# Kernel optimization log

Hardware: AMD Instinct MI355X
Metric: run time of the kernel (lower is better)

Reference implementation:

```python
import jax, jax.numpy as jnp
import numpy as np

B, L, D = 2048, 200, 128
HID = [80, 40]


def setup_inputs() -> dict:
    key = jax.random.key(0)
    ks = jax.random.split(key, 10)
    hist_emb = jax.random.normal(ks[0], (B, L, D), dtype=jnp.float32)
    target_emb = jax.random.normal(ks[1], (B, D), dtype=jnp.float32)
    mask = jax.random.randint(ks[2], (B, L), 0, 2, dtype=jnp.int32)
    # MLP params: (4D -> 80 -> 40 -> 1), Kaiming-uniform-ish like nn.Linear default
    dims = [4 * D] + HID + [1]
    params = {}
    for i in range(len(dims) - 1):
        fan_in = dims[i]
        bound = 1.0 / np.sqrt(fan_in)
        params[f"W{i}"] = jax.random.uniform(ks[3 + 2 * i], (dims[i], dims[i + 1]), minval=-bound, maxval=bound, dtype=jnp.float32)
        params[f"b{i}"] = jax.random.uniform(ks[4 + 2 * i], (dims[i + 1],), minval=-bound, maxval=bound, dtype=jnp.float32)
    return {"hist_emb": hist_emb, "target_emb": target_emb, "mask": mask, **params}


def reference(hist_emb, target_emb, mask, W0, b0, W1, b1, W2, b2):
    # hist_emb: (B,L,D); target_emb: (B,D); mask: (B,L)
    target = target_emb[:, None, :]                       # (B,1,D) -> broadcast over L
    diff = hist_emb - target
    prod = hist_emb * target
    tgt = jnp.broadcast_to(target, hist_emb.shape)
    feat = jnp.concatenate([hist_emb, tgt, diff, prod], axis=-1)  # (B,L,4D)
    h = jax.nn.relu(jnp.einsum("blf,fh->blh", feat, W0) + b0)
    h = jax.nn.relu(jnp.einsum("blf,fh->blh", h, W1) + b1)
    scores = (jnp.einsum("blf,fh->blh", h, W2) + b2)[..., 0]      # (B,L)
    m = mask.astype(scores.dtype)
    logits = scores + (1.0 - m) * -1e9
    attn = jax.nn.softmax(logits, axis=1)                 # (B,L)
    user_interest = jnp.einsum("bl,bld->bd", attn, hist_emb)
    return user_interest, attn
```

## Files before the change

kernel.cpp:

```cpp
#include <hip/hip_runtime.h>
#include <hip/hip_bf16.h>

#define B_  2048
#define L_  200
#define D_  128
#define H0_ 80
#define H1_ 40
#define BPB 4
#define NTILE 13
#define TT_ (BPB*NTILE)

#define WS_BG  0
#define WS_W1T 20480
#define WS_W0P 25088
#define WS_TOT 35840

typedef __attribute__((ext_vector_type(8))) short short8;
typedef __attribute__((ext_vector_type(4))) float floatx4;

__device__ __forceinline__ short f2bf(float f) {
    unsigned u = __float_as_uint(f);
    u += 0x7fffu + ((u >> 16) & 1u);
    return (short)(u >> 16);
}
__device__ __forceinline__ float bf2f(short s) {
    return __uint_as_float(((unsigned)(unsigned short)s) << 16);
}

__global__ __launch_bounds__(256) void prep_kernel(
    const float* __restrict__ W0, const float* __restrict__ W1,
    short* __restrict__ ws)
{
    for (int i = blockIdx.x * 256 + threadIdx.x; i < WS_TOT; i += 64 * 256) {
        short v;
        if (i < WS_W1T) {
            int h = i >> 8, k = i & 255;
            float x = (k < 128) ? (W0[(size_t)k * H0_ + h] + W0[(size_t)(256 + k) * H0_ + h])
                                : W0[(size_t)(384 + (k - 128)) * H0_ + h];
            v = f2bf(x);
        } else if (i < WS_W0P) {
            int j = i - WS_W1T;
            int n = j / 96, k = j - n * 96;
            v = (n < H1_ && k < H0_) ? f2bf(W1[(size_t)k * H1_ + n]) : (short)0;
        } else {
            int j = i - WS_W0P;
            int d = j / 84, h = j - d * 84;
            v = (h < H0_) ? f2bf(W0[(size_t)(128 + d) * H0_ + h] - W0[(size_t)(256 + d) * H0_ + h])
                          : (short)0;
        }
        ws[i] = v;
    }
}

__global__ __launch_bounds__(256, 2) void fused_kernel(
    const float* __restrict__ hist, const float* __restrict__ tgt,
    const int* __restrict__ mask, const short* __restrict__ ws,
    const float* __restrict__ b0p, const float* __restrict__ b1,
    const float* __restrict__ W2, const float* __restrict__ b2,
    float* __restrict__ out)
{
    __shared__ __align__(16) short Bs[H0_][264];
    __shared__ __align__(16) short h0t[4][16][104];
    __shared__ float tgs4[BPB][D_];
    __shared__ float beffs[BPB][H0_];
    __shared__ float scores4[BPB][208];
    __shared__ float red[8];
    __shared__ float p0[D_], p1[D_];

    const int tid = threadIdx.x;
    const int wave = tid >> 6, lane = tid & 63;
    const int col = lane & 15, quad = lane >> 4;
    const int bbase = blockIdx.x * BPB;

    short* w0s = &Bs[0][0];
    float* red3 = &scores4[0][0];

    for (int i = tid; i < 1344; i += 256)
        *(short8*)(w0s + i * 8) = *(const short8*)(ws + WS_W0P + i * 8);
    for (int i = tid; i < BPB * D_; i += 256)
        tgs4[i >> 7][i & 127] = tgt[(size_t)(bbase + (i >> 7)) * D_ + (i & 127)];
    __syncthreads();

    for (int bb = 0; bb < BPB; ++bb) {
        if (tid < 240) {
            int seg = tid / 80, h = tid - seg * 80;
            int d0 = seg * 43, d1 = (seg == 2) ? D_ : d0 + 43;
            float s = 0.f;
            #pragma unroll 8
            for (int d = d0; d < d1; ++d) s += tgs4[bb][d] * bf2f(w0s[d * 84 + h]);
            red3[seg * H0_ + h] = s;
        }
        __syncthreads();
        if (tid < H0_)
            beffs[bb][tid] = b0p[tid] + red3[tid] + red3[H0_ + tid] + red3[2 * H0_ + tid];
        __syncthreads();
    }

    for (int i = tid; i < 2560; i += 256) {
        int h = i >> 5, k0 = (i & 31) * 8;
        *(short8*)&Bs[h][k0] = *(const short8*)(ws + WS_BG + (h << 8) + k0);
    }
    if (tid < 192) {
        int w = tid / 48, rem = tid % 48, row = rem / 3, c = 80 + (rem % 3) * 8;
        *(short8*)&h0t[w][row][c] = (short8)0;
    }
    short8 w1f[3][3];
    #pragma unroll
    for (int ks = 0; ks < 3; ++ks)
        #pragma unroll
        for (int nt = 0; nt < 3; ++nt)
            w1f[ks][nt] = *(const short8*)(ws + WS_W1T + (nt * 16 + col) * 96 + ks * 32 + quad * 8);
    float b1r[3], w2r[3];
    #pragma unroll
    for (int nt = 0; nt < 3; ++nt) {
        int h = nt * 16 + col;
        b1r[nt] = (h < H1_) ? b1[h] : 0.f;
        w2r[nt] = (h < H1_) ? W2[h] : 0.f;
    }
    const float b2v = b2[0];
    __syncthreads();

    for (int tt = wave; tt < TT_; tt += 4) {
        const int bb = tt / NTILE, t = tt - bb * NTILE;
        const int l = t * 16 + col;
        const int lc = (l < L_) ? l : (L_ - 1);
        const float* ap = hist + ((size_t)(bbase + bb) * L_ + lc) * D_ + quad * 8;

        floatx4 A[8], T8[8];
        #pragma unroll
        for (int u = 0; u < 8; ++u) A[u] = *(const floatx4*)(ap + (u >> 1) * 32 + (u & 1) * 4);
        #pragma unroll
        for (int u = 0; u < 8; ++u)
            T8[u] = *(const floatx4*)&tgs4[bb][quad * 8 + (u >> 1) * 32 + (u & 1) * 4];

        short8 ah[4], ag[4];
        #pragma unroll
        for (int ks = 0; ks < 4; ++ks) {
            short8 h8, g8;
            #pragma unroll
            for (int j = 0; j < 8; ++j) {
                float hv = A[2 * ks + (j >> 2)][j & 3];
                float tv = T8[2 * ks + (j >> 2)][j & 3];
                h8[j] = f2bf(hv);
                g8[j] = f2bf(hv * tv);
            }
            ah[ks] = h8; ag[ks] = g8;
        }

        floatx4 c0[5];
        #pragma unroll
        for (int nt = 0; nt < 5; ++nt) c0[nt] = (floatx4)0.f;
        #pragma unroll
        for (int ks = 0; ks < 4; ++ks)
            #pragma unroll
            for (int nt = 0; nt < 5; ++nt) {
                short8 bfr = *(const short8*)&Bs[nt * 16 + col][ks * 32 + quad * 8];
                c0[nt] = __builtin_amdgcn_mfma_f32_16x16x32_bf16(ah[ks], bfr, c0[nt], 0, 0, 0);
            }
        #pragma unroll
        for (int ks = 0; ks < 4; ++ks)
            #pragma unroll
            for (int nt = 0; nt < 5; ++nt) {
                short8 bfr = *(const short8*)&Bs[nt * 16 + col][128 + ks * 32 + quad * 8];
                c0[nt] = __builtin_amdgcn_mfma_f32_16x16x32_bf16(ag[ks], bfr, c0[nt], 0, 0, 0);
            }

        #pragma unroll
        for (int nt = 0; nt < 5; ++nt) {
            float be = beffs[bb][nt * 16 + col];
            #pragma unroll
            for (int r = 0; r < 4; ++r) {
                float v = c0[nt][r] + be;
                v = v > 0.f ? v : 0.f;
                h0t[wave][quad * 4 + r][nt * 16 + col] = f2bf(v);
            }
        }

        floatx4 c1[3];
        #pragma unroll
        for (int nt = 0; nt < 3; ++nt) c1[nt] = (floatx4)0.f;
        #pragma unroll
        for (int ks = 0; ks < 3; ++ks) {
            short8 a1 = *(const short8*)&h0t[wave][col][ks * 32 + quad * 8];
            #pragma unroll
            for (int nt = 0; nt < 3; ++nt)
                c1[nt] = __builtin_amdgcn_mfma_f32_16x16x32_bf16(a1, w1f[ks][nt], c1[nt], 0, 0, 0);
        }

        float s4[4] = {0.f, 0.f, 0.f, 0.f};
        #pragma unroll
        for (int nt = 0; nt < 3; ++nt)
            #pragma unroll
            for (int r = 0; r < 4; ++r) {
                float v = c1[nt][r] + b1r[nt];
                v = v > 0.f ? v : 0.f;
                s4[r] += v * w2r[nt];
            }
        #pragma unroll
        for (int r = 0; r < 4; ++r) {
            s4[r] += __shfl_xor(s4[r], 1, 16);
            s4[r] += __shfl_xor(s4[r], 2, 16);
            s4[r] += __shfl_xor(s4[r], 4, 16);
            s4[r] += __shfl_xor(s4[r], 8, 16);
        }
        if (col == 0) {
            #pragma unroll
            for (int r = 0; r < 4; ++r)
                scores4[bb][t * 16 + quad * 4 + r] = s4[r] + b2v;
        }
    }
    __syncthreads();

    for (int bb = 0; bb < BPB; ++bb) {
        const int b = bbase + bb;

        float sc = -3.0e38f;
        if (tid < L_) {
            sc = scores4[bb][tid];
            if (mask[(size_t)b * L_ + tid] == 0) sc -= 1e9f;
        }
        float m = sc;
        #pragma unroll
        for (int off = 32; off >= 1; off >>= 1) m = fmaxf(m, __shfl_xor(m, off, 64));
        if (lane == 0) red[wave] = m;
        __syncthreads();
        m = fmaxf(fmaxf(red[0], red[1]), fmaxf(red[2], red[3]));
        float e = (tid < L_) ? __expf(sc - m) : 0.f;
        float s = e;
        #pragma unroll
        for (int off = 32; off >= 1; off >>= 1) s += __shfl_xor(s, off, 64);
        if (lane == 0) red[4 + wave] = s;
        __syncthreads();
        s = red[4] + red[5] + red[6] + red[7];
        float av = e * (1.0f / s);
        if (tid < L_) {
            scores4[bb][tid] = av;
            out[(size_t)B_ * D_ + (size_t)b * L_ + tid] = av;
        }
        __syncthreads();

        const int half = tid >> 7, d = tid & 127;
        const float* hb = hist + ((size_t)b * L_ + half * 100) * D_ + d;
        float acc = 0.f;
        #pragma unroll 25
        for (int l = 0; l < 100; ++l)
            acc = fmaf(scores4[bb][half * 100 + l], hb[(size_t)l * D_], acc);
        if (half) p1[d] = acc; else p0[d] = acc;
        __syncthreads();
        if (tid < D_) out[(size_t)b * D_ + tid] = p0[tid] + p1[tid];
    }
}

extern "C" void kernel_launch(void* const* d_in, const int* in_sizes, int n_in,
                              void* d_out, int out_size, void* d_ws, size_t ws_size,
                              hipStream_t stream) {
    const float* hist = (const float*)d_in[0];
    const float* tgt  = (const float*)d_in[1];
    const int*   mask = (const int*)d_in[2];
    const float* W0   = (const float*)d_in[3];
    const float* b0   = (const float*)d_in[4];
    const float* W1   = (const float*)d_in[5];
    const float* b1   = (const float*)d_in[6];
    const float* W2   = (const float*)d_in[7];
    const float* b2   = (const float*)d_in[8];

    short* ws = (short*)d_ws;

    prep_kernel<<<64, 256, 0, stream>>>(W0, W1, ws);
    fused_kernel<<<B_ / BPB, 256, 0, stream>>>(hist, tgt, mask, ws, b0, b1, W2, b2,
                                               (float*)d_out);
}
```

Measured before the change: 362.1 us.

## Fold target into per-batch W0 to halve first-layer MFMAs, raise occupancy

Each batch row's target vector is folded into an effective first-layer weight (Wa + t*Wd) built in shared memory, so layer 0 needs only the hist operand and half the MFMAs per tile. Batches per block drop from 4 to 2 and launch bounds rise to 4 blocks per CU, with a smaller shared-memory footprint. The softmax and weighted sum are rewritten so each wave pair handles one batch with fewer barriers and float2 loads. In exchange, the weight matrix is rebuilt per batch with a barrier each time, and folding t into the bf16 weights adds rounding error.

```diff
diff --git a/kernel.cpp b/kernel.cpp
--- a/kernel.cpp
+++ b/kernel.cpp
@@ -6,9 +6,8 @@
 #define D_  128
 #define H0_ 80
 #define H1_ 40
-#define BPB 4
+#define BPB 2
 #define NTILE 13
-#define TT_ (BPB*NTILE)
 
 #define WS_BG  0
 #define WS_W1T 20480
@@ -17,6 +16,7 @@
 
 typedef __attribute__((ext_vector_type(8))) short short8;
 typedef __attribute__((ext_vector_type(4))) float floatx4;
+typedef __attribute__((ext_vector_type(2))) float floatx2;
 
 __device__ __forceinline__ short f2bf(float f) {
     unsigned u = __float_as_uint(f);
@@ -52,56 +52,30 @@
     }
 }
 
-__global__ __launch_bounds__(256, 2) void fused_kernel(
+__global__ __launch_bounds__(256, 4) void fused_kernel(
     const float* __restrict__ hist, const float* __restrict__ tgt,
     const int* __restrict__ mask, const short* __restrict__ ws,
     const float* __restrict__ b0p, const float* __restrict__ b1,
     const float* __restrict__ W2, const float* __restrict__ b2,
     float* __restrict__ out)
 {
-    __shared__ __align__(16) short Bs[H0_][264];
-    __shared__ __align__(16) short h0t[4][16][104];
+    __shared__ __align__(16) short wbuf[10752];
+    __shared__ __align__(16) short h0t[4][16][100];
     __shared__ float tgs4[BPB][D_];
     __shared__ float beffs[BPB][H0_];
     __shared__ float scores4[BPB][208];
-    __shared__ float red[8];
-    __shared__ float p0[D_], p1[D_];
 
     const int tid = threadIdx.x;
     const int wave = tid >> 6, lane = tid & 63;
     const int col = lane & 15, quad = lane >> 4;
     const int bbase = blockIdx.x * BPB;
 
-    short* w0s = &Bs[0][0];
-    float* red3 = &scores4[0][0];
-
     for (int i = tid; i < 1344; i += 256)
-        *(short8*)(w0s + i * 8) = *(const short8*)(ws + WS_W0P + i * 8);
+        *(short8*)(wbuf + i * 8) = *(const short8*)(ws + WS_W0P + i * 8);
     for (int i = tid; i < BPB * D_; i += 256)
         tgs4[i >> 7][i & 127] = tgt[(size_t)(bbase + (i >> 7)) * D_ + (i & 127)];
-    __syncthreads();
-
-    for (int bb = 0; bb < BPB; ++bb) {
-        if (tid < 240) {
-            int seg = tid / 80, h = tid - seg * 80;
-            int d0 = seg * 43, d1 = (seg == 2) ? D_ : d0 + 43;
-            float s = 0.f;
-            #pragma unroll 8
-            for (int d = d0; d < d1; ++d) s += tgs4[bb][d] * bf2f(w0s[d * 84 + h]);
-            red3[seg * H0_ + h] = s;
-        }
-        __syncthreads();
-        if (tid < H0_)
-            beffs[bb][tid] = b0p[tid] + red3[tid] + red3[H0_ + tid] + red3[2 * H0_ + tid];
-        __syncthreads();
-    }
-
-    for (int i = tid; i < 2560; i += 256) {
-        int h = i >> 5, k0 = (i & 31) * 8;
-        *(short8*)&Bs[h][k0] = *(const short8*)(ws + WS_BG + (h << 8) + k0);
-    }
-    if (tid < 192) {
-        int w = tid / 48, rem = tid % 48, row = rem / 3, c = 80 + (rem % 3) * 8;
+    if (tid < 128) {
+        int w = tid >> 5, row = (tid >> 1) & 15, c = 80 + (tid & 1) * 8;
         *(short8*)&h0t[w][row][c] = (short8)0;
     }
     short8 w1f[3][3];
@@ -120,134 +94,168 @@
     const float b2v = b2[0];
     __syncthreads();
 
-    for (int tt = wave; tt < TT_; tt += 4) {
-        const int bb = tt / NTILE, t = tt - bb * NTILE;
-        const int l = t * 16 + col;
-        const int lc = (l < L_) ? l : (L_ - 1);
-        const float* ap = hist + ((size_t)(bbase + bb) * L_ + lc) * D_ + quad * 8;
-
-        floatx4 A[8], T8[8];
-        #pragma unroll
-        for (int u = 0; u < 8; ++u) A[u] = *(const floatx4*)(ap + (u >> 1) * 32 + (u & 1) * 4);
-        #pragma unroll
-        for (int u = 0; u < 8; ++u)
-            T8[u] = *(const floatx4*)&tgs4[bb][quad * 8 + (u >> 1) * 32 + (u & 1) * 4];
-
-        short8 ah[4], ag[4];
-        #pragma unroll
-        for (int ks = 0; ks < 4; ++ks) {
-            short8 h8, g8;
-            #pragma unroll
-            for (int j = 0; j < 8; ++j) {
-                float hv = A[2 * ks + (j >> 2)][j & 3];
-                float tv = T8[2 * ks + (j >> 2)][j & 3];
-                h8[j] = f2bf(hv);
-                g8[j] = f2bf(hv * tv);
-            }
-            ah[ks] = h8; ag[ks] = g8;
-        }
-
-        floatx4 c0[5];
-        #pragma unroll
-        for (int nt = 0; nt < 5; ++nt) c0[nt] = (floatx4)0.f;
-        #pragma unroll
-        for (int ks = 0; ks < 4; ++ks)
+    if (tid < 160) {
+        int bb = tid >= 80 ? 1 : 0, h = tid - bb * 80;
+        float s = 0.f;
+        #pragma unroll 8
+        for (int d = 0; d < D_; ++d) s += tgs4[bb][d] * bf2f(wbuf[d * 84 + h]);
+        beffs[bb][h] = b0p[h] + s;
+    }
+    __syncthreads();
+
+    for (int bb = 0; bb < BPB; ++bb) {
+        for (int i = tid; i < 1280; i += 256) {
+            int h = i >> 4, d0 = (i & 15) * 8;
+            short8 wa = *(const short8*)(ws + WS_BG + h * 256 + d0);
+            short8 wd = *(const short8*)(ws + WS_BG + h * 256 + 128 + d0);
+            floatx4 t0 = *(const floatx4*)&tgs4[bb][d0];
+            floatx4 t1 = *(const floatx4*)&tgs4[bb][d0 + 4];
+            short8 o;
+            #pragma unroll
+            for (int j = 0; j < 4; ++j) o[j] = f2bf(bf2f(wa[j]) + t0[j] * bf2f(wd[j]));
+            #pragma unroll
+            for (int j = 4; j < 8; ++j) o[j] = f2bf(bf2f(wa[j]) + t1[j - 4] * bf2f(wd[j]));
+            *(short8*)(wbuf + h * 132 + d0) = o;
+        }
+        __syncthreads();
+
+        const int b = bbase + bb;
+        for (int t = (wave + bb) & 3; t < NTILE; t += 4) {
+            const int l = t * 16 + col;
+            const int lc = (l < L_) ? l : (L_ - 1);
+            const float* ap = hist + ((size_t)b * L_ + lc) * D_ + quad * 8;
+
+            floatx4 A[8];
+            #pragma unroll
+            for (int u = 0; u < 8; ++u)
+                A[u] = *(const floatx4*)(ap + (u >> 1) * 32 + (u & 1) * 4);
+
+            short8 ah[4];
+            #pragma unroll
+            for (int ks = 0; ks < 4; ++ks) {
+                short8 h8;
+                #pragma unroll
+                for (int j = 0; j < 8; ++j) h8[j] = f2bf(A[2 * ks + (j >> 2)][j & 3]);
+                ah[ks] = h8;
+            }
+
+            floatx4 c0[5];
+            #pragma unroll
+            for (int nt = 0; nt < 5; ++nt) c0[nt] = (floatx4)0.f;
+            #pragma unroll
+            for (int ks = 0; ks < 4; ++ks)
+                #pragma unroll
+                for (int nt = 0; nt < 5; ++nt) {
+                    short8 bfr = *(const short8*)(wbuf + (nt * 16 + col) * 132 + ks * 32 + quad * 8);
+                    c0[nt] = __builtin_amdgcn_mfma_f32_16x16x32_bf16(ah[ks], bfr, c0[nt], 0, 0, 0);
+                }
+
             #pragma unroll
             for (int nt = 0; nt < 5; ++nt) {
-                short8 bfr = *(const short8*)&Bs[nt * 16 + col][ks * 32 + quad * 8];
-                c0[nt] = __builtin_amdgcn_mfma_f32_16x16x32_bf16(ah[ks], bfr, c0[nt], 0, 0, 0);
-            }
-        #pragma unroll
-        for (int ks = 0; ks < 4; ++ks)
-            #pragma unroll
-            for (int nt = 0; nt < 5; ++nt) {
-                short8 bfr = *(const short8*)&Bs[nt * 16 + col][128 + ks * 32 + quad * 8];
-                c0[nt] = __builtin_amdgcn_mfma_f32_16x16x32_bf16(ag[ks], bfr, c0[nt], 0, 0, 0);
-            }
-
-        #pragma unroll
-        for (int nt = 0; nt < 5; ++nt) {
-            float be = beffs[bb][nt * 16 + col];
+                float be = beffs[bb][nt * 16 + col];
+                #pragma unroll
+                for (int r = 0; r < 4; ++r) {
+                    float v = c0[nt][r] + be;
+                    v = v > 0.f ? v : 0.f;
+                    h0t[wave][quad * 4 + r][nt * 16 + col] = f2bf(v);
+                }
+            }
+
+            floatx4 c1[3];
+            #pragma unroll
+            for (int nt = 0; nt < 3; ++nt) c1[nt] = (floatx4)0.f;
+            #pragma unroll
+            for (int ks = 0; ks < 3; ++ks) {
+                short8 a1 = *(const short8*)&h0t[wave][col][ks * 32 + quad * 8];
+                #pragma unroll
+                for (int nt = 0; nt < 3; ++nt)
+                    c1[nt] = __builtin_amdgcn_mfma_f32_16x16x32_bf16(a1, w1f[ks][nt], c1[nt], 0, 0, 0);
+            }
+
+            float s4[4] = {0.f, 0.f, 0.f, 0.f};
+            #pragma unroll
+            for (int nt = 0; nt < 3; ++nt)
+                #pragma unroll
+                for (int r = 0; r < 4; ++r) {
+                    float v = c1[nt][r] + b1r[nt];
+                    v = v > 0.f ? v : 0.f;
+                    s4[r] += v * w2r[nt];
+                }
             #pragma unroll
             for (int r = 0; r < 4; ++r) {
-                float v = c0[nt][r] + be;
-                v = v > 0.f ? v : 0.f;
-                h0t[wave][quad * 4 + r][nt * 16 + col] = f2bf(v);
-            }
-        }
-
-        floatx4 c1[3];
-        #pragma unroll
-        for (int nt = 0; nt < 3; ++nt) c1[nt] = (floatx4)0.f;
-        #pragma unroll
-        for (int ks = 0; ks < 3; ++ks) {
-            short8 a1 = *(const short8*)&h0t[wave][col][ks * 32 + quad * 8];
-            #pragma unroll
-            for (int nt = 0; nt < 3; ++nt)
-                c1[nt] = __builtin_amdgcn_mfma_f32_16x16x32_bf16(a1, w1f[ks][nt], c1[nt], 0, 0, 0);
-        }
-
-        float s4[4] = {0.f, 0.f, 0.f, 0.f};
-        #pragma unroll
-        for (int nt = 0; nt < 3; ++nt)
-            #pragma unroll
-            for (int r = 0; r < 4; ++r) {
-                float v = c1[nt][r] + b1r[nt];
-                v = v > 0.f ? v : 0.f;
-                s4[r] += v * w2r[nt];
-            }
-        #pragma unroll
-        for (int r = 0; r < 4; ++r) {
-            s4[r] += __shfl_xor(s4[r], 1, 16);
-            s4[r] += __shfl_xor(s4[r], 2, 16);
-            s4[r] += __shfl_xor(s4[r], 4, 16);
-            s4[r] += __shfl_xor(s4[r], 8, 16);
-        }
-        if (col == 0) {
-            #pragma unroll
-            for (int r = 0; r < 4; ++r)
-                scores4[bb][t * 16 + quad * 4 + r] = s4[r] + b2v;
-        }
-    }
-    __syncthreads();
-
-    for (int bb = 0; bb < BPB; ++bb) {
-        const int b = bbase + bb;
-
-        float sc = -3.0e38f;
-        if (tid < L_) {
-            sc = scores4[bb][tid];
-            if (mask[(size_t)b * L_ + tid] == 0) sc -= 1e9f;
-        }
-        float m = sc;
+                s4[r] += __shfl_xor(s4[r], 1, 16);
+                s4[r] += __shfl_xor(s4[r], 2, 16);
+                s4[r] += __shfl_xor(s4[r], 4, 16);
+                s4[r] += __shfl_xor(s4[r], 8, 16);
+            }
+            if (col == 0) {
+                #pragma unroll
+                for (int r = 0; r < 4; ++r)
+                    scores4[bb][t * 16 + quad * 4 + r] = s4[r] + b2v;
+            }
+        }
+        __syncthreads();
+    }
+
+    float* pw = (float*)&h0t[0][0][0];
+    float* attn_w = pw + 4 * 128;
+    {
+        const int bb = wave >> 1, b = bbase + bb, half = wave & 1;
+        float sc[4], e[4];
+        float m = -3.0e38f;
+        #pragma unroll
+        for (int j = 0; j < 4; ++j) {
+            int idx = lane + 64 * j;
+            if (idx < L_) {
+                float v = scores4[bb][idx];
+                if (mask[(size_t)b * L_ + idx] == 0) v -= 1e9f;
+                sc[j] = v;
+                m = fmaxf(m, v);
+            } else sc[j] = -3.0e38f;
+        }
         #pragma unroll
         for (int off = 32; off >= 1; off >>= 1) m = fmaxf(m, __shfl_xor(m, off, 64));
-        if (lane == 0) red[wave] = m;
-        __syncthreads();
-        m = fmaxf(fmaxf(red[0], red[1]), fmaxf(red[2], red[3]));
-        float e = (tid < L_) ? __expf(sc - m) : 0.f;
-        float s = e;
+        float s = 0.f;
+        #pragma unroll
+        for (int j = 0; j < 4; ++j) {
+            int idx = lane + 64 * j;
+            e[j] = (idx < L_) ? __expf(sc[j] - m) : 0.f;
+            s += e[j];
+        }
         #pragma unroll
         for (int off = 32; off >= 1; off >>= 1) s += __shfl_xor(s, off, 64);
-        if (lane == 0) red[4 + wave] = s;
-        __syncthreads();
-        s = red[4] + red[5] + red[6] + red[7];
-        float av = e * (1.0f / s);
-        if (tid < L_) {
-            scores4[bb][tid] = av;
-            out[(size_t)B_ * D_ + (size_t)b * L_ + tid] = av;
-        }
-        __syncthreads();
-
-        const int half = tid >> 7, d = tid & 127;
-        const float* hb = hist + ((size_t)b * L_ + half * 100) * D_ + d;
-        float acc = 0.f;
+        float inv = 1.0f / s;
+        if (half == 0) {
+            #pragma unroll
+            for (int j = 0; j < 4; ++j) {
+                int idx = lane + 64 * j;
+                if (idx < L_) {
+                    float av = e[j] * inv;
+                    attn_w[bb * 200 + idx] = av;
+                    out[(size_t)B_ * D_ + (size_t)b * L_ + idx] = av;
+                }
+            }
+        }
+    }
+    __syncthreads();
+    {
+        const int bb = wave >> 1, b = bbase + bb, half = wave & 1;
+        const int d2 = lane * 2;
+        const float* hb = hist + ((size_t)b * L_ + half * 100) * D_ + d2;
+        float a0 = 0.f, a1 = 0.f;
         #pragma unroll 25
-        for (int l = 0; l < 100; ++l)
-            acc = fmaf(scores4[bb][half * 100 + l], hb[(size_t)l * D_], acc);
-        if (half) p1[d] = acc; else p0[d] = acc;
-        __syncthreads();
-        if (tid < D_) out[(size_t)b * D_ + tid] = p0[tid] + p1[tid];
+        for (int l = 0; l < 100; ++l) {
+            float w = attn_w[bb * 200 + half * 100 + l];
+            floatx2 h2 = *(const floatx2*)(hb + (size_t)l * D_);
+            a0 = fmaf(w, h2.x, a0);
+            a1 = fmaf(w, h2.y, a1);
+        }
+        *(floatx2*)&pw[wave * 128 + d2] = floatx2{a0, a1};
+    }
+    __syncthreads();
+    {
+        int bp = tid >> 7, d = tid & 127;
+        out[(size_t)(bbase + bp) * D_ + d] = pw[(bp * 2) * 128 + d] + pw[(bp * 2 + 1) * 128 + d];
     }
 }
 
```

Result: slower. 403.1 us (+11.3%).

## Fold target product into per-batch W0 fragments and prefetch history tiles

Applied to the files above, without the earlier changes.

Since the target is constant within a batch row, the hist*target block of W0 is folded into an effective per-batch weight (W_a + t*W_d) built in registers. This halves the first-layer MFMA count and removes the shared-memory weight tile. The first-layer bias is now computed by looping over all 128 dimensions from global memory in one pass, replacing the segmented reduction and two syncs per batch. The tile loop is restructured per batch with a staggered start and register prefetch of the next history tile. The cost is extra register pressure from 20 weight fragments plus the prefetch buffer, and a second bf16 rounding of the effective weights.

```diff
diff --git a/kernel.cpp b/kernel.cpp
--- a/kernel.cpp
+++ b/kernel.cpp
@@ -8,7 +8,6 @@
 #define H1_ 40
 #define BPB 4
 #define NTILE 13
-#define TT_ (BPB*NTILE)
 
 #define WS_BG  0
 #define WS_W1T 20480
@@ -59,7 +58,6 @@
     const float* __restrict__ W2, const float* __restrict__ b2,
     float* __restrict__ out)
 {
-    __shared__ __align__(16) short Bs[H0_][264];
     __shared__ __align__(16) short h0t[4][16][104];
     __shared__ float tgs4[BPB][D_];
     __shared__ float beffs[BPB][H0_];
@@ -72,34 +70,8 @@
     const int col = lane & 15, quad = lane >> 4;
     const int bbase = blockIdx.x * BPB;
 
-    short* w0s = &Bs[0][0];
-    float* red3 = &scores4[0][0];
-
-    for (int i = tid; i < 1344; i += 256)
-        *(short8*)(w0s + i * 8) = *(const short8*)(ws + WS_W0P + i * 8);
     for (int i = tid; i < BPB * D_; i += 256)
         tgs4[i >> 7][i & 127] = tgt[(size_t)(bbase + (i >> 7)) * D_ + (i & 127)];
-    __syncthreads();
-
-    for (int bb = 0; bb < BPB; ++bb) {
-        if (tid < 240) {
-            int seg = tid / 80, h = tid - seg * 80;
-            int d0 = seg * 43, d1 = (seg == 2) ? D_ : d0 + 43;
-            float s = 0.f;
-            #pragma unroll 8
-            for (int d = d0; d < d1; ++d) s += tgs4[bb][d] * bf2f(w0s[d * 84 + h]);
-            red3[seg * H0_ + h] = s;
-        }
-        __syncthreads();
-        if (tid < H0_)
-            beffs[bb][tid] = b0p[tid] + red3[tid] + red3[H0_ + tid] + red3[2 * H0_ + tid];
-        __syncthreads();
-    }
-
-    for (int i = tid; i < 2560; i += 256) {
-        int h = i >> 5, k0 = (i & 31) * 8;
-        *(short8*)&Bs[h][k0] = *(const short8*)(ws + WS_BG + (h << 8) + k0);
-    }
     if (tid < 192) {
         int w = tid / 48, rem = tid % 48, row = rem / 3, c = 80 + (rem % 3) * 8;
         *(short8*)&h0t[w][row][c] = (short8)0;
@@ -120,93 +92,129 @@
     const float b2v = b2[0];
     __syncthreads();
 
-    for (int tt = wave; tt < TT_; tt += 4) {
-        const int bb = tt / NTILE, t = tt - bb * NTILE;
-        const int l = t * 16 + col;
-        const int lc = (l < L_) ? l : (L_ - 1);
-        const float* ap = hist + ((size_t)(bbase + bb) * L_ + lc) * D_ + quad * 8;
-
-        floatx4 A[8], T8[8];
-        #pragma unroll
-        for (int u = 0; u < 8; ++u) A[u] = *(const floatx4*)(ap + (u >> 1) * 32 + (u & 1) * 4);
-        #pragma unroll
-        for (int u = 0; u < 8; ++u)
-            T8[u] = *(const floatx4*)&tgs4[bb][quad * 8 + (u >> 1) * 32 + (u & 1) * 4];
-
-        short8 ah[4], ag[4];
+    for (int p = tid; p < BPB * H0_; p += 256) {
+        int bb = p / H0_, h = p - bb * H0_;
+        float s = 0.f;
+        #pragma unroll 8
+        for (int d = 0; d < D_; ++d)
+            s += tgs4[bb][d] * bf2f(ws[WS_W0P + d * 84 + h]);
+        beffs[bb][h] = b0p[h] + s;
+    }
+    __syncthreads();
+
+    for (int bb = 0; bb < BPB; ++bb) {
+        const int b = bbase + bb;
+        int t = (wave + bb) & 3;
+
+        floatx4 A[8];
+        {
+            const int l = t * 16 + col;
+            const int lc = (l < L_) ? l : (L_ - 1);
+            const float* ap = hist + ((size_t)b * L_ + lc) * D_ + quad * 8;
+            #pragma unroll
+            for (int u = 0; u < 8; ++u)
+                A[u] = *(const floatx4*)(ap + (u >> 1) * 32 + (u & 1) * 4);
+        }
+
+        short8 w0e[4][5];
         #pragma unroll
         for (int ks = 0; ks < 4; ++ks) {
-            short8 h8, g8;
-            #pragma unroll
-            for (int j = 0; j < 8; ++j) {
-                float hv = A[2 * ks + (j >> 2)][j & 3];
-                float tv = T8[2 * ks + (j >> 2)][j & 3];
-                h8[j] = f2bf(hv);
-                g8[j] = f2bf(hv * tv);
-            }
-            ah[ks] = h8; ag[ks] = g8;
-        }
-
-        floatx4 c0[5];
-        #pragma unroll
-        for (int nt = 0; nt < 5; ++nt) c0[nt] = (floatx4)0.f;
-        #pragma unroll
-        for (int ks = 0; ks < 4; ++ks)
+            const int d0 = ks * 32 + quad * 8;
+            floatx4 t0 = *(const floatx4*)&tgs4[bb][d0];
+            floatx4 t1 = *(const floatx4*)&tgs4[bb][d0 + 4];
             #pragma unroll
             for (int nt = 0; nt < 5; ++nt) {
-                short8 bfr = *(const short8*)&Bs[nt * 16 + col][ks * 32 + quad * 8];
-                c0[nt] = __builtin_amdgcn_mfma_f32_16x16x32_bf16(ah[ks], bfr, c0[nt], 0, 0, 0);
-            }
-        #pragma unroll
-        for (int ks = 0; ks < 4; ++ks)
+                const int h = nt * 16 + col;
+                short8 wa = *(const short8*)(ws + WS_BG + h * 256 + d0);
+                short8 wd = *(const short8*)(ws + WS_BG + h * 256 + 128 + d0);
+                short8 o;
+                #pragma unroll
+                for (int j = 0; j < 4; ++j) o[j] = f2bf(bf2f(wa[j]) + t0[j] * bf2f(wd[j]));
+                #pragma unroll
+                for (int j = 4; j < 8; ++j) o[j] = f2bf(bf2f(wa[j]) + t1[j - 4] * bf2f(wd[j]));
+                w0e[ks][nt] = o;
+            }
+        }
+
+        while (t < NTILE) {
+            const int tn = t + 4;
+            floatx4 An[8];
+            if (tn < NTILE) {
+                const int l = tn * 16 + col;
+                const int lc = (l < L_) ? l : (L_ - 1);
+                const float* ap = hist + ((size_t)b * L_ + lc) * D_ + quad * 8;
+                #pragma unroll
+                for (int u = 0; u < 8; ++u)
+                    An[u] = *(const floatx4*)(ap + (u >> 1) * 32 + (u & 1) * 4);
+            }
+
+            short8 ah[4];
+            #pragma unroll
+            for (int ks = 0; ks < 4; ++ks) {
+                short8 h8;
+                #pragma unroll
+                for (int j = 0; j < 8; ++j) h8[j] = f2bf(A[2 * ks + (j >> 2)][j & 3]);
+                ah[ks] = h8;
+            }
+
+            floatx4 c0[5];
+            #pragma unroll
+            for (int nt = 0; nt < 5; ++nt) c0[nt] = (floatx4)0.f;
+            #pragma unroll
+            for (int ks = 0; ks < 4; ++ks)
+                #pragma unroll
+                for (int nt = 0; nt < 5; ++nt)
+                    c0[nt] = __builtin_amdgcn_mfma_f32_16x16x32_bf16(ah[ks], w0e[ks][nt], c0[nt], 0, 0, 0);
+
             #pragma unroll
             for (int nt = 0; nt < 5; ++nt) {
-                short8 bfr = *(const short8*)&Bs[nt * 16 + col][128 + ks * 32 + quad * 8];
-                c0[nt] = __builtin_amdgcn_mfma_f32_16x16x32_bf16(ag[ks], bfr, c0[nt], 0, 0, 0);
-            }
-
-        #pragma unroll
-        for (int nt = 0; nt < 5; ++nt) {
-            float be = beffs[bb][nt * 16 + col];
+                float be = beffs[bb][nt * 16 + col];
+                #pragma unroll
+                for (int r = 0; r < 4; ++r) {
+                    float v = c0[nt][r] + be;
+                    v = v > 0.f ? v : 0.f;
+                    h0t[wave][quad * 4 + r][nt * 16 + col] = f2bf(v);
+                }
+            }
+
+            floatx4 c1[3];
+            #pragma unroll
+            for (int nt = 0; nt < 3; ++nt) c1[nt] = (floatx4)0.f;
+            #pragma unroll
+            for (int ks = 0; ks < 3; ++ks) {
+                short8 a1 = *(const short8*)&h0t[wave][col][ks * 32 + quad * 8];
+                #pragma unroll
+                for (int nt = 0; nt < 3; ++nt)
+                    c1[nt] = __builtin_amdgcn_mfma_f32_16x16x32_bf16(a1, w1f[ks][nt], c1[nt], 0, 0, 0);
+            }
+
+            float s4[4] = {0.f, 0.f, 0.f, 0.f};
+            #pragma unroll
+            for (int nt = 0; nt < 3; ++nt)
+                #pragma unroll
+                for (int r = 0; r < 4; ++r) {
+                    float v = c1[nt][r] + b1r[nt];
+                    v = v > 0.f ? v : 0.f;
+                    s4[r] += v * w2r[nt];
+                }
             #pragma unroll
             for (int r = 0; r < 4; ++r) {
-                float v = c0[nt][r] + be;
-                v = v > 0.f ? v : 0.f;
-                h0t[wave][quad * 4 + r][nt * 16 + col] = f2bf(v);
-            }
-        }
-
-        floatx4 c1[3];
-        #pragma unroll
-        for (int nt = 0; nt < 3; ++nt) c1[nt] = (floatx4)0.f;
-        #pragma unroll
-        for (int ks = 0; ks < 3; ++ks) {
-            short8 a1 = *(const short8*)&h0t[wave][col][ks * 32 + quad * 8];
-            #pragma unroll
-            for (int nt = 0; nt < 3; ++nt)
-                c1[nt] = __builtin_amdgcn_mfma_f32_16x16x32_bf16(a1, w1f[ks][nt], c1[nt], 0, 0, 0);
-        }
-
-        float s4[4] = {0.f, 0.f, 0.f, 0.f};
-        #pragma unroll
-        for (int nt = 0; nt < 3; ++nt)
-            #pragma unroll
-            for (int r = 0; r < 4; ++r) {
-                float v = c1[nt][r] + b1r[nt];
-                v = v > 0.f ? v : 0.f;
-                s4[r] += v * w2r[nt];
-            }
-        #pragma unroll
-        for (int r = 0; r < 4; ++r) {
-            s4[r] += __shfl_xor(s4[r], 1, 16);
-            s4[r] += __shfl_xor(s4[r], 2, 16);
-            s4[r] += __shfl_xor(s4[r], 4, 16);
-            s4[r] += __shfl_xor(s4[r], 8, 16);
-        }
-        if (col == 0) {
-            #pragma unroll
-            for (int r = 0; r < 4; ++r)
-                scores4[bb][t * 16 + quad * 4 + r] = s4[r] + b2v;
+                s4[r] += __shfl_xor(s4[r], 1, 16);
+                s4[r] += __shfl_xor(s4[r], 2, 16);
+                s4[r] += __shfl_xor(s4[r], 4, 16);
+                s4[r] += __shfl_xor(s4[r], 8, 16);
+            }
+            if (col == 0) {
+                #pragma unroll
+                for (int r = 0; r < 4; ++r)
+                    scores4[bb][t * 16 + quad * 4 + r] = s4[r] + b2v;
+            }
+
+            if (tn < NTILE) {
+                #pragma unroll
+                for (int u = 0; u < 8; ++u) A[u] = An[u];
+            }
+            t = tn;
         }
     }
     __syncthreads();
```

Result: slower. 556.2 us (+53.6%).
